# Kernel optimization log

Measured on AMD Instinct MI355X. Metric: run time of the kernel, lower is better.

Reference implementation:

```python
import jax, jax.numpy as jnp
import numpy as np

ODE_UNFOLDS = 6
MOTOR_SIZE = 3
EPS = 1e-8

def _conv(x, w, b, stride):
    y = jax.lax.conv_general_dilated(x, w, (stride, stride), 'VALID',
                                     dimension_numbers=('NCHW', 'OIHW', 'NCHW'))
    return jax.nn.relu(y + b[None, :, None, None])

def _conv_head(x, w1, b1, w2, b2, w3, b3, w4, b4, w5, b5, fc_w, fc_b):
    # x: [B, T, 3, 66, 200] -> features [B, T, 128]
    B, T = x.shape[0], x.shape[1]
    h = x.reshape(B * T, *x.shape[2:])
    h = _conv(h, w1, b1, 2)  # [BT,24,31,98]
    h = _conv(h, w2, b2, 2)  # [BT,36,14,47]
    h = _conv(h, w3, b3, 2)  # [BT,48,5,22]
    h = _conv(h, w4, b4, 1)  # [BT,64,3,20]
    h = _conv(h, w5, b5, 1)  # [BT,64,1,18]
    h = h.reshape(B * T, -1)
    h = jax.nn.relu(h @ fc_w + fc_b)
    return h.reshape(B, T, -1)

def _ltc_step(inputs, v, s_mu, s_sigma, s_w, s_erev, mu, sigma, w, erev, gleak, vleak, cm):
    # inputs: [B,S], v: [B,N]
    # sensory synapse activations (constant over the ODE unfolds)
    s_act = s_w * jax.nn.sigmoid((inputs[:, :, None] - s_mu) * s_sigma)  # [B,S,N]
    w_num_s = jnp.sum(s_act * s_erev, axis=1)  # [B,N]
    w_den_s = jnp.sum(s_act, axis=1)           # [B,N]
    cm_t = cm * ODE_UNFOLDS  # cm / (elapsed=1 / ode_unfolds)
    for _ in range(ODE_UNFOLDS):
        w_act = w * jax.nn.sigmoid((v[:, :, None] - mu) * sigma)  # [B,N,N]
        w_num = jnp.sum(w_act * erev, axis=1) + w_num_s
        w_den = jnp.sum(w_act, axis=1) + w_den_s
        v = (cm_t * v + gleak * vleak + w_num) / (cm_t + gleak + w_den + EPS)
    return v[:, :MOTOR_SIZE], v

def reference(x, w1, b1, w2, b2, w3, b3, w4, b4, w5, b5, fc_w, fc_b,
              s_mu, s_sigma, s_w, s_erev, mu, sigma, w, erev, gleak, vleak, cm):
    y = _conv_head(x, w1, b1, w2, b2, w3, b3, w4, b4, w5, b5, fc_w, fc_b)  # [B,T,128]
    B, T, _ = y.shape
    N = mu.shape[0]
    v0 = jnp.zeros((B, N), dtype=y.dtype)

    def step(v, inp):
        out, v = _ltc_step(inp, v, s_mu, s_sigma, s_w, s_erev, mu, sigma, w, erev, gleak, vleak, cm)
        return v, out

    _, outs = jax.lax.scan(step, v0, jnp.swapaxes(y, 0, 1))  # outs: [T,B,3]
    return jnp.swapaxes(outs, 0, 1)  # [B,T,3]

def setup_inputs() -> dict:
    key = jax.random.key(0)
    ks = jax.random.split(key, 24)
    d = {}
    d['x'] = jax.random.normal(ks[0], (32, 16, 3, 66, 200), jnp.float32)
    shapes = [((24, 3, 5, 5), (24,)), ((36, 24, 5, 5), (36,)), ((48, 36, 5, 5), (48,)),
              ((64, 48, 3, 3), (64,)), ((64, 64, 3, 3), (64,))]
    for i, (ws, bs) in enumerate(shapes):
        d[f'w{i+1}'] = jax.random.normal(ks[1 + i], ws, jnp.float32) * 0.05
        d[f'b{i+1}'] = jnp.zeros(bs, jnp.float32)
    d['fc_w'] = jax.random.normal(ks[6], (1152, 128), jnp.float32) * 0.05
    d['fc_b'] = jnp.zeros((128,), jnp.float32)
    S, N = 128, 64
    d['s_mu'] = jax.random.normal(ks[7], (S, N), jnp.float32) * 0.3 + 0.3
    d['s_sigma'] = jax.random.uniform(ks[8], (S, N), jnp.float32, 3.0, 8.0)
    d['s_w'] = jax.random.uniform(ks[9], (S, N), jnp.float32, 0.001, 1.0)
    d['s_erev'] = jnp.sign(jax.random.normal(ks[10], (S, N), jnp.float32))
    d['mu'] = jax.random.normal(ks[11], (N, N), jnp.float32) * 0.3 + 0.3
    d['sigma'] = jax.random.uniform(ks[12], (N, N), jnp.float32, 3.0, 8.0)
    d['w'] = jax.random.uniform(ks[13], (N, N), jnp.float32, 0.001, 1.0)
    d['erev'] = jnp.sign(jax.random.normal(ks[14], (N, N), jnp.float32))
    d['gleak'] = jax.random.uniform(ks[15], (N,), jnp.float32, 0.001, 1.0)
    d['vleak'] = jax.random.uniform(ks[16], (N,), jnp.float32, -0.2, 0.2)
    d['cm'] = jax.random.uniform(ks[17], (N,), jnp.float32, 0.4, 0.6)
    return d
```

## Files before the change

kernel.cpp:

```cpp
#include <hip/hip_runtime.h>
#include <hip/hip_bf16.h>


typedef _Float16 f16;
typedef _Float16 f16x8 __attribute__((ext_vector_type(8)));
typedef _Float16 f16x4 __attribute__((ext_vector_type(4)));
typedef float    f32x4 __attribute__((ext_vector_type(4)));
typedef unsigned int u32;

static __device__ __forceinline__ float sigmoidf_fast(float x) {
    return __builtin_amdgcn_rcpf(1.0f + __expf(-x));
}


__global__ __launch_bounds__(256)
void wpack1_kernel(const float* __restrict__ w1, f16* __restrict__ Wpk1)
{
    int idx = blockIdx.x * 256 + threadIdx.x;
    if (idx >= 32 * 136) return;
    int co = idx / 136;
    int kk = idx % 136;
    float v = 0.0f;
    if (co < 24 && kk < 120) {
        int p = kk >> 3, jj = kk & 7;
        int kh = p / 3, kwp = p % 3;
        int kws = jj >> 2, ci = jj & 3;
        int kw = 2 * kwp + kws;
        if (kw < 5 && ci < 3)
            v = w1[(((size_t)co * 3 + ci) * 5 + kh) * 5 + kw];
    }
    Wpk1[idx] = (f16)v;
}

__global__ __launch_bounds__(512)
void conv1_mfma(const float* __restrict__ x, const f16* __restrict__ Wpk1,
                const float* __restrict__ b1, f16* __restrict__ h1T)
{
    __shared__ __align__(16) f16 img[52800];
    __shared__ __align__(16) f16 Wl[4352];

    int m    = blockIdx.x;
    int tid  = threadIdx.x;
    int lane = tid & 63;
    int wv   = tid >> 6;
    int col  = lane & 15;
    int row4 = lane >> 4;

    for (int u = tid; u < 544; u += 512)
        *(uint4*)((char*)Wl + (size_t)u * 16) =
            *(const uint4*)((const char*)Wpk1 + (size_t)u * 16);

    const float* xb = x + (size_t)m * 39600;
    for (int u = tid; u < 13200; u += 512) {
        float a = xb[u], b = xb[13200 + u], c = xb[26400 + u];
        f16x4 pk = { (f16)a, (f16)b, (f16)c, (f16)0.0f };
        *(f16x4*)(&img[(size_t)u * 4]) = pk;
    }
    __syncthreads();

    f16x8 af[2][4];
    #pragma unroll
    for (int Mt = 0; Mt < 2; ++Mt)
        #pragma unroll
        for (int t = 0; t < 4; ++t)
            af[Mt][t] = *(const f16x8*)((const char*)Wl +
                           (Mt * 16 + col) * 272 + t * 64 + row4 * 16);

    int rowB[4], kwpv[4];
    #pragma unroll
    for (int t = 0; t < 4; ++t) {
        int p = 4 * t + row4; if (p > 14) p = 14;
        rowB[t] = (p / 3) * 1600;
        kwpv[t] = (p % 3) * 16;
    }

    float bvv[2][4];
    #pragma unroll
    for (int Mt = 0; Mt < 2; ++Mt)
        #pragma unroll
        for (int i = 0; i < 4; ++i) {
            int co = Mt * 16 + row4 * 4 + i;
            bvv[Mt][i] = (co < 24) ? b1[co] : 0.0f;
        }

    const char* ic = (const char*)img;
    for (int it = 0; it < 24; ++it) {
        int s = wv + it * 8;
        if (s * 16 >= 3038) continue;
        int px = s * 16 + col;
        bool pv = (px < 3038);
        int pc = pv ? px : 3037;
        int ho = pc / 98;
        int wo = pc - ho * 98;
        int base = ho * 3200 + wo * 16;

        f32x4 a0 = {0.f,0.f,0.f,0.f}, a1 = {0.f,0.f,0.f,0.f};
        #pragma unroll
        for (int t = 0; t < 4; ++t) {
            f16x8 xf = *(const f16x8*)(ic + base + rowB[t] + kwpv[t]);
            a0 = __builtin_amdgcn_mfma_f32_16x16x32_f16(af[0][t], xf, a0, 0, 0, 0);
            a1 = __builtin_amdgcn_mfma_f32_16x16x32_f16(af[1][t], xf, a1, 0, 0, 0);
        }

        if (pv) {
            size_t rowbase = ((size_t)m * 31 + ho) * 296;
            int par = (wo & 1) * 49, wh = wo >> 1;
            int j0 = (row4 & 1) * 4;
            {
                int c8 = row4 >> 1;
                f16x4 pk = { (f16)fmaxf(a0[0] + bvv[0][0], 0.0f),
                             (f16)fmaxf(a0[1] + bvv[0][1], 0.0f),
                             (f16)fmaxf(a0[2] + bvv[0][2], 0.0f),
                             (f16)fmaxf(a0[3] + bvv[0][3], 0.0f) };
                int sl = c8 * 98 + par + wh;
                *(f16x4*)(h1T + (rowbase + sl) * 8 + j0) = pk;
            }
            if (row4 < 2) {
                f16x4 pk = { (f16)fmaxf(a1[0] + bvv[1][0], 0.0f),
                             (f16)fmaxf(a1[1] + bvv[1][1], 0.0f),
                             (f16)fmaxf(a1[2] + bvv[1][2], 0.0f),
                             (f16)fmaxf(a1[3] + bvv[1][3], 0.0f) };
                int sl = 2 * 98 + par + wh;
                *(f16x4*)(h1T + (rowbase + sl) * 8 + j0) = pk;
            }
        }
    }
}

__global__ __launch_bounds__(256)
void wpack_kernel(const float* __restrict__ w2, f16* __restrict__ Wpk)
{
    int idx = blockIdx.x * 256 + threadIdx.x;
    if (idx >= 48 * 616) return;
    int co = idx / 616;
    int kk = idx % 616;
    float v = 0.0f;
    if (kk < 608 && co < 36) {
        int c = kk >> 3, j = kk & 7;
        if (c < 75) {
            int pq = c / 3, c8 = c - 3 * pq;
            int kh = pq / 5, kw = pq - 5 * kh;
            int ci = c8 * 8 + j;
            v = w2[(((size_t)co * 24 + ci) * 5 + kh) * 5 + kw];
        }
    }
    Wpk[idx] = (f16)v;
}

__global__ __launch_bounds__(256)
void wpack3_kernel(const float* __restrict__ w3, f16* __restrict__ Wpk3)
{
    int idx = blockIdx.x * 256 + threadIdx.x;
    if (idx >= 48 * 1032) return;
    int co = idx / 1032;
    int kk = idx % 1032;
    float v = 0.0f;
    if (kk < 1024) {
        int c = kk >> 3, j = kk & 7;
        int pq = c / 5, c8 = c - 5 * pq;
        if (pq < 25) {
            int kh = pq / 5, kw = pq - 5 * kh;
            int ci = c8 * 8 + j;
            if (ci < 36)
                v = w3[(((size_t)co * 36 + ci) * 5 + kh) * 5 + kw];
        }
    }
    Wpk3[idx] = (f16)v;
}

__global__ __launch_bounds__(384)
void conv2_mfma(const f16* __restrict__ h1T, const f16* __restrict__ Wpk,
                const float* __restrict__ b2, f16* __restrict__ h2f)
{
    __shared__ __align__(16) f16 img[73408];
    __shared__ u32 lutS[76];

    int m    = blockIdx.x;
    int tid  = threadIdx.x;
    int lane = tid & 63;
    int wv   = tid >> 6;
    int ct   = wv >> 1;
    int sh   = wv & 1;
    int row4 = lane >> 4;
    int col  = lane & 15;

    if (tid < 76) {
        int c = tid; u32 v = 0;
        if (c < 75) {
            int pq = c / 3, c8 = c - 3 * pq;
            int kh = pq / 5, kw = pq - 5 * kh;
            u32 ofs = (u32)(c8 * 98 + (kw & 1) * 49 + (kw >> 1));
            v = ((u32)(kh * 4736) << 8) | ofs;
        }
        lutS[c] = v;
    }

    f16x8 af[19];
    {
        const char* wb = (const char*)Wpk + (size_t)(ct * 16 + col) * 1232 + row4 * 16;
        #pragma unroll
        for (int t = 0; t < 19; ++t)
            af[t] = *(const f16x8*)(wb + t * 64);
    }

    {
        const char* g = (const char*)(h1T + (size_t)m * 73408);
        for (int u = tid; u < 9176; u += 384)
            *(uint4*)((char*)img + (size_t)u * 16) = *(const uint4*)(g + (size_t)u * 16);
    }

    float bv[4];
    #pragma unroll
    for (int i = 0; i < 4; ++i) {
        int co = ct * 16 + row4 * 4 + i;
        bv[i] = (co < 36) ? b2[co] : 0.0f;
    }
    int c8o  = ct * 2 + (row4 >> 1);
    int hsel = (row4 & 1) * 4;

    __syncthreads();

    const char* ic = (const char*)img;
    for (int it = 0; it < 7; ++it) {
        int rbase[3], valid[3], hov[3], wov[3];
        #pragma unroll
        for (int si = 0; si < 3; ++si) {
            int tile = sh * 21 + it * 3 + si;
            int px   = tile * 16 + col;
            valid[si] = (px < 658);
            int pc = valid[si] ? px : 657;
            int ho = pc / 47;
            int wo = pc - 47 * ho;
            rbase[si] = ho * 9472 + wo * 16;
            hov[si] = ho; wov[si] = wo;
        }

        f32x4 acc0 = {0.f,0.f,0.f,0.f}, acc1 = {0.f,0.f,0.f,0.f}, acc2 = {0.f,0.f,0.f,0.f};
        #pragma unroll
        for (int t = 0; t < 19; ++t) {
            u32 lv   = lutS[4 * t + row4];
            int rowb = (int)(lv >> 8);
            int boff = (int)(lv & 255) << 4;
            f16x8 a = af[t];
            {
                f16x8 xf = *(const f16x8*)(ic + rbase[0] + rowb + boff);
                acc0 = __builtin_amdgcn_mfma_f32_16x16x32_f16(a, xf, acc0, 0, 0, 0);
            }
            {
                f16x8 xf = *(const f16x8*)(ic + rbase[1] + rowb + boff);
                acc1 = __builtin_amdgcn_mfma_f32_16x16x32_f16(a, xf, acc1, 0, 0, 0);
            }
            {
                f16x8 xf = *(const f16x8*)(ic + rbase[2] + rowb + boff);
                acc2 = __builtin_amdgcn_mfma_f32_16x16x32_f16(a, xf, acc2, 0, 0, 0);
            }
        }

        #pragma unroll
        for (int si = 0; si < 3; ++si) {
            f32x4 a = (si == 0) ? acc0 : (si == 1) ? acc1 : acc2;
            if (valid[si] && c8o < 5) {
                int wo = wov[si], ho = hov[si];
                f16x4 pk;
                #pragma unroll
                for (int i = 0; i < 4; ++i) pk[i] = (f16)fmaxf(a[i] + bv[i], 0.0f);
                int sl = c8o * 47 + (wo & 1) * 24 + (wo >> 1);
                *(f16x4*)(h2f + ((size_t)m * 3374 + (size_t)ho * 241 + sl) * 8 + hsel) = pk;
            }
        }
    }
}

__global__ __launch_bounds__(384)
void conv3_mfma(const f16* __restrict__ h2f, const f16* __restrict__ Wpk3,
                const float* __restrict__ b3, float* __restrict__ h3)
{
    __shared__ __align__(16) f16 Wl[48 * 1032];
    __shared__ __align__(16) f16 img[3374 * 8];
    __shared__ u32 lut[128];

    int m    = blockIdx.x;
    int tid  = threadIdx.x;
    int lane = tid & 63;
    int wv   = tid >> 6;
    int ct   = wv >> 1;
    int sh   = wv & 1;
    int row4 = lane >> 4;
    int col  = lane & 15;

    if (tid < 128) {
        int c  = tid;
        int pq = c / 5, c8 = c - 5 * pq;
        int kh = pq / 5, kw = pq - 5 * kh;
        lut[c] = ((u32)(kh * 3856) << 8) |
                 (u32)(c8 * 47 + (kw & 1) * 24 + (kw >> 1));
    }
    for (int u = tid; u < 6192; u += 384)
        *(uint4*)((char*)Wl + (size_t)u * 16) =
            *(const uint4*)((const char*)Wpk3 + (size_t)u * 16);
    {
        const char* g = (const char*)(h2f + (size_t)m * 3374 * 8);
        for (int u = tid; u < 3374; u += 384)
            *(uint4*)((char*)img + (size_t)u * 16) = *(const uint4*)(g + (size_t)u * 16);
    }
    __syncthreads();

    int rb[4], wo16[4], valid[4], hov[4], wov[4];
    int nsi = 4 - sh;
    #pragma unroll
    for (int si = 0; si < 4; ++si) {
        int s  = 4 * sh + si;
        int px = 16 * s + col;
        valid[si] = (si < nsi) && (px < 110);
        int pc = px < 110 ? px : 109;
        int ho = pc / 22, wo = pc - 22 * ho;
        rb[si]   = ho * 7712;
        wo16[si] = wo * 16;
        hov[si]  = ho; wov[si] = wo;
    }

    float bv[4];
    #pragma unroll
    for (int i = 0; i < 4; ++i) bv[i] = b3[ct * 16 + row4 * 4 + i];

    int Abase = (ct * 16 + col) * 2064 + row4 * 16;
    const char* Wc = (const char*)Wl;
    const char* ic = (const char*)img;

    f32x4 a0 = {0.f,0.f,0.f,0.f}, a1 = {0.f,0.f,0.f,0.f};
    f32x4 a2 = {0.f,0.f,0.f,0.f}, a3 = {0.f,0.f,0.f,0.f};
    #pragma unroll 8
    for (int t = 0; t < 32; ++t) {
        u32 lv     = lut[4 * t + row4];
        int rowoff = (int)(lv >> 8);
        int boff   = (int)(lv & 255) << 4;
        f16x8 af = *(const f16x8*)(Wc + Abase + 64 * t);
        {
            f16x8 xf = *(const f16x8*)(ic + rb[0] + rowoff + boff + wo16[0]);
            a0 = __builtin_amdgcn_mfma_f32_16x16x32_f16(af, xf, a0, 0, 0, 0);
        }
        {
            f16x8 xf = *(const f16x8*)(ic + rb[1] + rowoff + boff + wo16[1]);
            a1 = __builtin_amdgcn_mfma_f32_16x16x32_f16(af, xf, a1, 0, 0, 0);
        }
        {
            f16x8 xf = *(const f16x8*)(ic + rb[2] + rowoff + boff + wo16[2]);
            a2 = __builtin_amdgcn_mfma_f32_16x16x32_f16(af, xf, a2, 0, 0, 0);
        }
        {
            f16x8 xf = *(const f16x8*)(ic + rb[3] + rowoff + boff + wo16[3]);
            a3 = __builtin_amdgcn_mfma_f32_16x16x32_f16(af, xf, a3, 0, 0, 0);
        }
    }

    int co0 = ct * 16 + row4 * 4;
    #pragma unroll
    for (int si = 0; si < 4; ++si) {
        if (!valid[si]) continue;
        f32x4 a = (si == 0) ? a0 : (si == 1) ? a1 : (si == 2) ? a2 : a3;
        float* op = h3 + (((size_t)m * 48 + co0) * 5 + hov[si]) * 22 + wov[si];
        #pragma unroll
        for (int i = 0; i < 4; ++i)
            op[(size_t)i * 110] = fmaxf(a[i] + bv[i], 0.0f);
    }
}

template<int CIN, int KH, int KW, int STRIDE, int CO_T, int WO_T>
__global__ __launch_bounds__(256)
void conv_tile_kernel(const float* __restrict__ in, const float* __restrict__ wt,
                      const float* __restrict__ bias, float* __restrict__ out,
                      int Cout, int Hin, int Win, int Hout, int Wout,
                      int n_cg, int n_wg, int M)
{
    constexpr int LOAD_W = (WO_T - 1) * STRIDE + KW;

    int bx = blockIdx.x;
    int cg = bx % n_cg;
    int gid = (bx / n_cg) * blockDim.x + threadIdx.x;
    int wg = gid % n_wg;
    int t  = gid / n_wg;
    int ho = t % Hout;
    int m  = t / Hout;
    if (m >= M) return;

    int wo0 = wg * WO_T;
    int co0 = cg * CO_T;

    const float* ip = in + ((size_t)(m * CIN) * Hin + (size_t)ho * STRIDE) * Win
                         + (size_t)wo0 * STRIDE;
    const float* wp = wt + (size_t)co0 * (CIN * KH * KW);

    float acc[CO_T][WO_T];
    #pragma unroll
    for (int c = 0; c < CO_T; ++c) {
        float b = bias[co0 + c];
        #pragma unroll
        for (int q = 0; q < WO_T; ++q) acc[c][q] = b;
    }

    #pragma unroll 1
    for (int ci = 0; ci < CIN; ++ci) {
        #pragma unroll
        for (int kh = 0; kh < KH; ++kh) {
            const float* row = ip + ((size_t)ci * Hin + kh) * Win;
            float xv[LOAD_W];
            #pragma unroll
            for (int l = 0; l < LOAD_W; ++l) xv[l] = row[l];
            const float* wrow = wp + (ci * KH + kh) * KW;
            #pragma unroll
            for (int c = 0; c < CO_T; ++c) {
                #pragma unroll
                for (int kw = 0; kw < KW; ++kw) {
                    float wv = wrow[c * (CIN * KH * KW) + kw];
                    #pragma unroll
                    for (int q = 0; q < WO_T; ++q)
                        acc[c][q] = fmaf(xv[q * STRIDE + kw], wv, acc[c][q]);
                }
            }
        }
    }

    #pragma unroll
    for (int c = 0; c < CO_T; ++c) {
        float* op = out + (((size_t)m * Cout + co0 + c) * Hout + ho) * Wout + wo0;
        #pragma unroll
        for (int q = 0; q < WO_T; ++q) {
            if (wo0 + q < Wout) op[q] = fmaxf(acc[c][q], 0.0f);
        }
    }
}

__global__ __launch_bounds__(256)
void fc_relu_kernel(const float* __restrict__ h, const float* __restrict__ w,
                    const float* __restrict__ b, float* __restrict__ out)
{
    __shared__ float hs[1152];
    __shared__ float part[8][32][4];
    int f   = blockIdx.x;
    int tid = threadIdx.x;
    int ks  = tid >> 5;
    int j4  = tid & 31;
    for (int k = tid; k < 1152; k += 256) hs[k] = h[(size_t)f * 1152 + k];
    __syncthreads();
    const float4* w4 = (const float4*)w;
    float4 acc = {0.f, 0.f, 0.f, 0.f};
    int k0 = ks * 144;
    #pragma unroll 4
    for (int kk = 0; kk < 144; ++kk) {
        int k = k0 + kk;
        float4 wv = w4[(size_t)k * 32 + j4];
        float hb = hs[k];
        acc.x = fmaf(wv.x, hb, acc.x);
        acc.y = fmaf(wv.y, hb, acc.y);
        acc.z = fmaf(wv.z, hb, acc.z);
        acc.w = fmaf(wv.w, hb, acc.w);
    }
    *(float4*)&part[ks][j4][0] = acc;
    __syncthreads();
    if (tid < 128) {
        int j = tid, jq = j >> 2, r = j & 3;
        float s = b[j];
        #pragma unroll
        for (int q = 0; q < 8; ++q) s += part[q][jq][r];
        out[(size_t)f * 128 + j] = fmaxf(s, 0.0f);
    }
}

__global__ __launch_bounds__(64)
void sensory_kernel(const float* __restrict__ feat,
                    const float* __restrict__ s_mu,
                    const float* __restrict__ s_sigma,
                    const float* __restrict__ s_w,
                    const float* __restrict__ s_erev,
                    float* __restrict__ wnum, float* __restrict__ wden)
{
    __shared__ float y[128];
    int bt = blockIdx.x;
    int n  = threadIdx.x;
    for (int s = n; s < 128; s += 64) y[s] = feat[bt * 128 + s];
    __syncthreads();
    float num = 0.0f, den = 0.0f;
    for (int s = 0; s < 128; ++s) {
        int o = s * 64 + n;
        float a = s_w[o] * sigmoidf_fast((y[s] - s_mu[o]) * s_sigma[o]);
        num = fmaf(a, s_erev[o], num);
        den += a;
    }
    wnum[bt * 64 + n] = num;
    wden[bt * 64 + n] = den;
}

__global__ __launch_bounds__(512)
void ltc_wave_kernel(const float* __restrict__ wnum_s,
                     const float* __restrict__ wden_s,
                     const float* __restrict__ mu, const float* __restrict__ sigma,
                     const float* __restrict__ w, const float* __restrict__ erev,
                     const float* __restrict__ gleak, const float* __restrict__ vleak,
                     const float* __restrict__ cm, float* __restrict__ out, int T)
{
    __shared__ float2 pnd[2][8][64];

    int b    = blockIdx.x;
    int tid  = threadIdx.x;
    int lane = tid & 63;
    int p    = tid >> 6;

    float musig[8], nsg[8], wv[8], wev[8];
    #pragma unroll
    for (int ii = 0; ii < 8; ++ii) {
        int o = (8 * p + ii) * 64 + lane;
        float sg = sigma[o];
        musig[ii] = mu[o] * sg;
        nsg[ii]   = -sg;
        float wl  = w[o];
        wv[ii]    = wl;
        wev[ii]   = wl * erev[o];
    }
    float gl   = gleak[lane];
    float glvl = gl * vleak[lane];
    float cmt  = cm[lane] * 6.0f;
    float v    = 0.0f;
    int   buf  = 0;

    for (int t = 0; t < T; ++t) {
        float ns = wnum_s[(b * T + t) * 64 + lane];
        float ds = wden_s[(b * T + t) * 64 + lane];
        #pragma unroll 1
        for (int u = 0; u < 6; ++u) {
            float num = 0.0f, den = 0.0f;
            #pragma unroll
            for (int ii = 0; ii < 8; ++ii) {
                float vi  = __shfl(v, 8 * p + ii);
                float arg = fmaf(vi, nsg[ii], musig[ii]);
                float e   = __expf(arg);
                float s   = __builtin_amdgcn_rcpf(1.0f + e);
                den = fmaf(wv[ii], s, den);
                num = fmaf(wev[ii], s, num);
            }
            pnd[buf][p][lane] = make_float2(num, den);
            __syncthreads();
            float wn = ns, wd = ds;
            #pragma unroll
            for (int q = 0; q < 8; ++q) {
                float2 pq = pnd[buf][q][lane];
                wn += pq.x; wd += pq.y;
            }
            v = (fmaf(cmt, v, glvl) + wn) *
                __builtin_amdgcn_rcpf(cmt + gl + wd + 1e-8f);
            buf ^= 1;
        }
        if (tid < 3) out[(b * T + t) * 3 + tid] = v;
    }
}

extern "C" void kernel_launch(void* const* d_in, const int* in_sizes, int n_in,
                              void* d_out, int out_size, void* d_ws, size_t ws_size,
                              hipStream_t stream)
{
    (void)in_sizes; (void)n_in; (void)out_size; (void)ws_size;

    const float* x    = (const float*)d_in[0];
    const float* w1   = (const float*)d_in[1];
    const float* b1   = (const float*)d_in[2];
    const float* w2   = (const float*)d_in[3];
    const float* b2   = (const float*)d_in[4];
    const float* w3   = (const float*)d_in[5];
    const float* b3   = (const float*)d_in[6];
    const float* w4   = (const float*)d_in[7];
    const float* b4   = (const float*)d_in[8];
    const float* w5   = (const float*)d_in[9];
    const float* b5   = (const float*)d_in[10];
    const float* fcw  = (const float*)d_in[11];
    const float* fcb  = (const float*)d_in[12];
    const float* smu  = (const float*)d_in[13];
    const float* ssig = (const float*)d_in[14];
    const float* sw   = (const float*)d_in[15];
    const float* serv = (const float*)d_in[16];
    const float* mu   = (const float*)d_in[17];
    const float* sig  = (const float*)d_in[18];
    const float* ww   = (const float*)d_in[19];
    const float* erev = (const float*)d_in[20];
    const float* gl   = (const float*)d_in[21];
    const float* vl   = (const float*)d_in[22];
    const float* cm   = (const float*)d_in[23];
    float* out = (float*)d_out;

    const int BT = 512;

    char* wsB = (char*)d_ws;
    size_t off = 0;
    f16*   h1T  = (f16*)(wsB + off); off += (size_t)512 * 31 * 2368 * 2;
    f16*   Wpk  = (f16*)(wsB + off); off += 65536;
    f16*   h2f  = (f16*)(wsB + off); off += (size_t)512 * 3374 * 16;
    f16*   Wpk3 = (f16*)(wsB + off); off += 48 * 1032 * 2;
    f16*   Wpk1 = (f16*)(wsB + off); off += 32 * 136 * 2;
    float* h3   = (float*)(wsB + off); off += (size_t)512 * 48 * 5 * 22 * 4;
    float* h4   = (float*)(wsB + off); off += (size_t)512 * 64 * 3 * 20 * 4;
    float* h5   = (float*)(wsB + off); off += (size_t)512 * 64 * 18 * 4;
    float* feat = (float*)(wsB + off); off += (size_t)BT * 128 * 4;
    float* wnum = (float*)(wsB + off); off += (size_t)BT * 64 * 4;
    float* wden = (float*)(wsB + off); off += (size_t)BT * 64 * 4;

    wpack1_kernel<<<(32 * 136 + 255) / 256, 256, 0, stream>>>(w1, Wpk1);
    wpack_kernel<<<(48 * 616 + 255) / 256, 256, 0, stream>>>(w2, Wpk);
    wpack3_kernel<<<(48 * 1032 + 255) / 256, 256, 0, stream>>>(w3, Wpk3);

    conv1_mfma<<<512, 512, 0, stream>>>(x, Wpk1, b1, h1T);
    conv2_mfma<<<512, 384, 0, stream>>>(h1T, Wpk, b2, h2f);
    conv3_mfma<<<512, 384, 0, stream>>>(h2f, Wpk3, b3, h3);

    {
        int n_cg = 16, n_wg = 5;
        int sp_threads = BT * 3 * n_wg;
        int grid = (sp_threads + 255) / 256 * n_cg;
        conv_tile_kernel<48, 3, 3, 1, 4, 4><<<grid, 256, 0, stream>>>(
            h3, w4, b4, h4, 64, 5, 22, 3, 20, n_cg, n_wg, BT);
    }
    {
        int n_cg = 16, n_wg = 6;
        int sp_threads = BT * 1 * n_wg;
        int grid = (sp_threads + 255) / 256 * n_cg;
        conv_tile_kernel<64, 3, 3, 1, 4, 3><<<grid, 256, 0, stream>>>(
            h4, w5, b5, h5, 64, 3, 20, 1, 18, n_cg, n_wg, BT);
    }
    fc_relu_kernel<<<512, 256, 0, stream>>>(h5, fcw, fcb, feat);
    sensory_kernel<<<BT, 64, 0, stream>>>(feat, smu, ssig, sw, serv, wnum, wden);
    ltc_wave_kernel<<<32, 512, 0, stream>>>(wnum, wden, mu, sig, ww, erev,
                                            gl, vl, cm, out, 16);
}
```

Measured before the change: 268.5 us.

## Split conv1 into two row-halves per image with vectorized loads

Conv1 now launches two blocks per image, each covering half of the output rows, so its shared-memory footprint shrinks from about 114KB to 56KB. This should let more blocks sit on each CU and double the grid to fill the GPU. The input staging switches to float4 loads. Weight fragments are read straight from global memory rather than through LDS, which drops the LDS copy and one barrier wait. The cost is some duplicated halo rows loaded by both halves.

```diff
diff --git a/kernel.cpp b/kernel.cpp
--- a/kernel.cpp
+++ b/kernel.cpp
@@ -36,35 +36,48 @@
 void conv1_mfma(const float* __restrict__ x, const f16* __restrict__ Wpk1,
                 const float* __restrict__ b1, f16* __restrict__ h1T)
 {
-    __shared__ __align__(16) f16 img[52800];
-    __shared__ __align__(16) f16 Wl[4352];
-
-    int m    = blockIdx.x;
+    __shared__ __align__(16) f16 img[35 * 200 * 4];
+
+    int blk  = blockIdx.x;
+    int m    = blk >> 1;
+    int hf   = blk & 1;
     int tid  = threadIdx.x;
     int lane = tid & 63;
     int wv   = tid >> 6;
     int col  = lane & 15;
     int row4 = lane >> 4;
 
-    for (int u = tid; u < 544; u += 512)
-        *(uint4*)((char*)Wl + (size_t)u * 16) =
-            *(const uint4*)((const char*)Wpk1 + (size_t)u * 16);
-
-    const float* xb = x + (size_t)m * 39600;
-    for (int u = tid; u < 13200; u += 512) {
-        float a = xb[u], b = xb[13200 + u], c = xb[26400 + u];
-        f16x4 pk = { (f16)a, (f16)b, (f16)c, (f16)0.0f };
-        *(f16x4*)(&img[(size_t)u * 4]) = pk;
-    }
-    __syncthreads();
+    int ho_base = hf * 16;
+    int r0      = 2 * ho_base;
+    int nrows   = hf ? 33 : 35;
+    int nho     = hf ? 15 : 16;
+    int npx     = nho * 98;
+    int ntile   = (npx + 15) >> 4;
+    int niter   = (ntile + 7) >> 3;
 
     f16x8 af[2][4];
     #pragma unroll
     for (int Mt = 0; Mt < 2; ++Mt)
         #pragma unroll
         for (int t = 0; t < 4; ++t)
-            af[Mt][t] = *(const f16x8*)((const char*)Wl +
+            af[Mt][t] = *(const f16x8*)((const char*)Wpk1 +
                            (Mt * 16 + col) * 272 + t * 64 + row4 * 16);
+
+    {
+        const float* p0 = x + (size_t)m * 39600 + (size_t)r0 * 200;
+        int n4 = (nrows * 200) >> 2;
+        for (int u4 = tid; u4 < n4; u4 += 512) {
+            float4 a = *(const float4*)(p0 + (size_t)u4 * 4);
+            float4 b = *(const float4*)(p0 + 13200 + (size_t)u4 * 4);
+            float4 c = *(const float4*)(p0 + 26400 + (size_t)u4 * 4);
+            f16x8 lo = { (f16)a.x, (f16)b.x, (f16)c.x, (f16)0.0f,
+                         (f16)a.y, (f16)b.y, (f16)c.y, (f16)0.0f };
+            f16x8 hi = { (f16)a.z, (f16)b.z, (f16)c.z, (f16)0.0f,
+                         (f16)a.w, (f16)b.w, (f16)c.w, (f16)0.0f };
+            *(f16x8*)(&img[(size_t)u4 * 16])     = lo;
+            *(f16x8*)(&img[(size_t)u4 * 16 + 8]) = hi;
+        }
+    }
 
     int rowB[4], kwpv[4];
     #pragma unroll
@@ -83,16 +96,18 @@
             bvv[Mt][i] = (co < 24) ? b1[co] : 0.0f;
         }
 
+    __syncthreads();
+
     const char* ic = (const char*)img;
-    for (int it = 0; it < 24; ++it) {
+    for (int it = 0; it < niter; ++it) {
         int s = wv + it * 8;
-        if (s * 16 >= 3038) continue;
+        if (s >= ntile) continue;
         int px = s * 16 + col;
-        bool pv = (px < 3038);
-        int pc = pv ? px : 3037;
-        int ho = pc / 98;
-        int wo = pc - ho * 98;
-        int base = ho * 3200 + wo * 16;
+        bool pv = (px < npx);
+        int pc = pv ? px : npx - 1;
+        int ho_l = pc / 98;
+        int wo   = pc - ho_l * 98;
+        int base = ho_l * 3200 + wo * 16;
 
         f32x4 a0 = {0.f,0.f,0.f,0.f}, a1 = {0.f,0.f,0.f,0.f};
         #pragma unroll
@@ -103,6 +118,7 @@
         }
 
         if (pv) {
+            int ho = ho_base + ho_l;
             size_t rowbase = ((size_t)m * 31 + ho) * 296;
             int par = (wo & 1) * 49, wh = wo >> 1;
             int j0 = (row4 & 1) * 4;
@@ -605,7 +621,7 @@
     wpack_kernel<<<(48 * 616 + 255) / 256, 256, 0, stream>>>(w2, Wpk);
     wpack3_kernel<<<(48 * 1032 + 255) / 256, 256, 0, stream>>>(w3, Wpk3);
 
-    conv1_mfma<<<512, 512, 0, stream>>>(x, Wpk1, b1, h1T);
+    conv1_mfma<<<1024, 512, 0, stream>>>(x, Wpk1, b1, h1T);
     conv2_mfma<<<512, 384, 0, stream>>>(h1T, Wpk, b2, h2f);
     conv3_mfma<<<512, 384, 0, stream>>>(h2f, Wpk3, b3, h3);
 
```

Result: faster. 260.2 us (-3.1%).
